# Kernel tuning notes

Measured on AMD Instinct MI355X. Metric: run time of the kernel, lower is better.

The kernel has to match this reference:

```python
import jax, jax.numpy as jnp
import numpy as np

EPS = 1e-5
PDIM, QKD, DIM = 64, 16, 256
SCALE = QKD ** -0.5


def setup_inputs() -> dict:
    key = jax.random.key(0)
    ks = jax.random.split(key, 13)
    B, H, W = 8, 64, 64
    return {
        "x": jax.random.normal(ks[0], (B, DIM, H, W), jnp.float32),
        "gn_g": jax.random.uniform(ks[1], (PDIM,), jnp.float32, 0.5, 1.5),
        "gn_b": jax.random.normal(ks[2], (PDIM,), jnp.float32) * 0.1,
        "qkv_w": jax.random.normal(ks[3], (2 * QKD + PDIM, PDIM), jnp.float32) * (PDIM ** -0.5),
        "qkv_bn_g": jax.random.uniform(ks[4], (2 * QKD + PDIM,), jnp.float32, 0.5, 1.5),
        "qkv_bn_b": jax.random.normal(ks[5], (2 * QKD + PDIM,), jnp.float32) * 0.1,
        "qkv_rm": jax.random.normal(ks[6], (2 * QKD + PDIM,), jnp.float32) * 0.1,
        "qkv_rv": jax.random.uniform(ks[7], (2 * QKD + PDIM,), jnp.float32, 0.5, 1.5),
        "proj_w": jax.random.normal(ks[8], (DIM, DIM), jnp.float32) * (DIM ** -0.5),
        "proj_bn_g": jax.random.uniform(ks[9], (DIM,), jnp.float32, 0.5, 1.5),
        "proj_bn_b": jax.random.normal(ks[10], (DIM,), jnp.float32) * 0.1,
        "proj_rm": jax.random.normal(ks[11], (DIM,), jnp.float32) * 0.1,
        "proj_rv": jax.random.uniform(ks[12], (DIM,), jnp.float32, 0.5, 1.5),
    }


def _bn(y, g, b, rm, rv):
    # inference BatchNorm over channel axis 1 of [B,C,H,W]
    inv = g / jnp.sqrt(rv + EPS)
    return y * inv[None, :, None, None] + (b - rm * inv)[None, :, None, None]


def reference(x, gn_g, gn_b, qkv_w, qkv_bn_g, qkv_bn_b, qkv_rm, qkv_rv,
              proj_w, proj_bn_g, proj_bn_b, proj_rm, proj_rv):
    B, C, H, W = x.shape
    x1, x2 = x[:, :PDIM], x[:, PDIM:]
    # GroupNorm with 1 group: normalize over (C,H,W) per sample
    mu = jnp.mean(x1, axis=(1, 2, 3), keepdims=True)
    var = jnp.var(x1, axis=(1, 2, 3), keepdims=True)
    x1n = (x1 - mu) / jnp.sqrt(var + EPS)
    x1n = x1n * gn_g[None, :, None, None] + gn_b[None, :, None, None]
    # qkv: 1x1 conv + BN
    qkv = jnp.einsum('bchw,oc->bohw', x1n, qkv_w)
    qkv = _bn(qkv, qkv_bn_g, qkv_bn_b, qkv_rm, qkv_rv)
    q, k, v = qkv[:, :QKD], qkv[:, QKD:2 * QKD], qkv[:, 2 * QKD:]
    N = H * W
    q = q.reshape(B, QKD, N)
    k = k.reshape(B, QKD, N)
    v = v.reshape(B, PDIM, N)
    attn = jnp.einsum('bcn,bcm->bnm', q, k) * SCALE  # [B,N,N]
    attn = jax.nn.softmax(attn, axis=-1)
    x1_attn = jnp.einsum('bcm,bnm->bcn', v, attn).reshape(B, PDIM, H, W)
    xc = jnp.concatenate([x1_attn, x2], axis=1)
    # proj: ReLU -> 1x1 conv -> BN
    y = jnp.einsum('bchw,oc->bohw', jax.nn.relu(xc), proj_w)
    return _bn(y, proj_bn_g, proj_bn_b, proj_rm, proj_rv)
```

## Files before the change

kernel.cpp:

```cpp
#include <hip/hip_runtime.h>
#include <hip/hip_bf16.h>

typedef __bf16 bf16;
typedef __bf16 bf16x4 __attribute__((ext_vector_type(4)));
typedef __bf16 bf16x8 __attribute__((ext_vector_type(8)));
typedef float  f32x16 __attribute__((ext_vector_type(16)));

#define MFMA32 __builtin_amdgcn_mfma_f32_32x32x16_bf16
#define EPSV 1e-5f
#define QSCALE 0.36067376022224085f

__device__ __forceinline__ f32x16 fzero16() {
  f32x16 z;
#pragma unroll
  for (int i = 0; i < 16; ++i) z[i] = 0.f;
  return z;
}

__global__ __launch_bounds__(256) void k_stats_partial(const float* __restrict__ x,
                                                       float* __restrict__ part) {
  const int b = blockIdx.x >> 5, k = blockIdx.x & 31;
  const float* p = x + (size_t)b * 256 * 4096 + k * 8192;
  const int t = threadIdx.x;
  float s = 0.f, q = 0.f;
#pragma unroll
  for (int j = 0; j < 8; ++j) {
    float4 v = ((const float4*)p)[t + j * 256];
    s += v.x + v.y + v.z + v.w;
    q += v.x * v.x + v.y * v.y + v.z * v.z + v.w * v.w;
  }
  __shared__ float ls[256], lq[256];
  ls[t] = s; lq[t] = q;
  __syncthreads();
  for (int off = 128; off > 0; off >>= 1) {
    if (t < off) { ls[t] += ls[t + off]; lq[t] += lq[t + off]; }
    __syncthreads();
  }
  if (t == 0) { part[blockIdx.x * 2] = ls[0]; part[blockIdx.x * 2 + 1] = lq[0]; }
}

__global__ __launch_bounds__(256) void k_stats_final(const float* __restrict__ part,
                                                     float* __restrict__ stats) {
  const int t = threadIdx.x, b = t >> 5, k = t & 31;
  float s = part[(b * 32 + k) * 2], q = part[(b * 32 + k) * 2 + 1];
  for (int off = 16; off > 0; off >>= 1) {
    s += __shfl_down(s, off, 32);
    q += __shfl_down(q, off, 32);
  }
  if (k == 0) {
    const float inv_n = 1.f / 262144.f;
    const float mu = s * inv_n;
    const float var = q * inv_n - mu * mu;
    stats[b * 2] = mu;
    stats[b * 2 + 1] = rsqrtf(var + EPSV);
  }
}

__global__ __launch_bounds__(256) void k_qkv(
    const float* __restrict__ x, const float* __restrict__ gn_g, const float* __restrict__ gn_b,
    const float* __restrict__ qkv_w, const float* __restrict__ bn_g, const float* __restrict__ bn_b,
    const float* __restrict__ bn_rm, const float* __restrict__ bn_rv,
    const float* __restrict__ stats,
    bf16* __restrict__ qw, bf16* __restrict__ kw, bf16* __restrict__ vw) {
  const int b = blockIdx.x >> 6, tile = blockIdx.x & 63;
  const int n0 = tile * 64, t = threadIdx.x;
  __shared__ float xn[64][68];
  __shared__ float W[64][96];
  __shared__ float beta_s[96];
  const float mu = stats[b * 2], rstd = stats[b * 2 + 1];
  {
    const int c = t >> 2, f = t & 3;
    const float A = rstd * gn_g[c], B = gn_b[c] - mu * A;
    const float* xr = x + ((size_t)b * 256 + c) * 4096 + n0;
#pragma unroll
    for (int j = 0; j < 4; ++j) {
      float4 v = ((const float4*)xr)[f * 4 + j];
      const int nb = f * 16 + j * 4;
      xn[c][nb + 0] = v.x * A + B; xn[c][nb + 1] = v.y * A + B;
      xn[c][nb + 2] = v.z * A + B; xn[c][nb + 3] = v.w * A + B;
    }
  }
  for (int oc = t; oc < 96 * 8; oc += 256) {
    const int o = oc >> 3, ch = (oc & 7) * 8;
    const float inv = bn_g[o] * rsqrtf(bn_rv[o] + EPSV);
    if (ch == 0) beta_s[o] = bn_b[o] - bn_rm[o] * inv;
    const float* wr = qkv_w + o * 64 + ch;
#pragma unroll
    for (int i = 0; i < 8; ++i) W[ch + i][o] = wr[i] * inv;
  }
  __syncthreads();
  const int o_l = t & 31, ng = t >> 5;
#pragma unroll 1
  for (int p = 0; p < 3; ++p) {
    const int o = p * 32 + o_l;
    float acc[8];
#pragma unroll
    for (int j = 0; j < 8; ++j) acc[j] = 0.f;
    for (int c = 0; c < 64; ++c) {
      const float wv = W[c][o];
      const float* xr = &xn[c][ng * 8];
#pragma unroll
      for (int j = 0; j < 8; ++j) acc[j] += wv * xr[j];
    }
    const float beta = beta_s[o];
    const int nb = n0 + ng * 8;
    if (p == 0) {
      if (o < 16) {
#pragma unroll
        for (int j = 0; j < 8; ++j)
          qw[((size_t)b * 4096 + nb + j) * 16 + o] = (bf16)((acc[j] + beta) * QSCALE);
      } else {
#pragma unroll
        for (int j = 0; j < 8; ++j)
          kw[((size_t)b * 4096 + nb + j) * 16 + (o - 16)] = (bf16)(acc[j] + beta);
      }
    } else {
      const int c = (p - 1) * 32 + o_l;
      bf16* vr = vw + ((size_t)b * 64 + c) * 4096 + nb;
#pragma unroll
      for (int q4 = 0; q4 < 2; ++q4) {
        bf16x4 pk;
        pk[0] = (bf16)(acc[q4 * 4 + 0] + beta); pk[1] = (bf16)(acc[q4 * 4 + 1] + beta);
        pk[2] = (bf16)(acc[q4 * 4 + 2] + beta); pk[3] = (bf16)(acc[q4 * 4 + 3] + beta);
        *(bf16x4*)(vr + q4 * 4) = pk;
      }
    }
  }
}

__global__ __launch_bounds__(1024, 4) void k_attn(
    const bf16* __restrict__ qw, const bf16* __restrict__ kw,
    const bf16* __restrict__ vw, const float* __restrict__ x,
    bf16* __restrict__ xc) {
  __shared__ __align__(16) char smem[81920];
  const int orig = blockIdx.x;
  const int wg = (orig & 7) * 32 + (orig >> 3);
  const int b = wg >> 5, qt = wg & 31;
  const int t = threadIdx.x;
  const int grp = t >> 8, tg = t & 255;
  const int wv4 = tg >> 6, l = t & 63, ln = l & 31, g = l >> 5;

  const bf16* qb = qw + (size_t)b * 4096 * 16;
  const char* kb = (const char*)(kw + (size_t)b * 4096 * 16);
  const bf16* vb = vw + (size_t)b * 64 * 4096;
  const int m0 = grp * 1024;

  char* kbase = smem + grp * 4096;
  char* vbase = smem + 16384 + grp * 16384;

  const char* ksrc = kb + (size_t)m0 * 32 + tg * 8;
  const int klds = (((tg >> 1) & 1) << 10) + ((tg >> 2) << 4) + ((tg & 1) << 3);
  const int vc = tg >> 2, vq = tg & 3;
  const bf16* vsrc = vb + (size_t)vc * 4096 + m0 + vq * 16;
  const int vswz = (vc & 15) * 8;

  const bf16x8 qf = *(const bf16x8*)(qb + (size_t)(qt * 128 + wv4 * 32 + ln) * 16 + g * 8);

  uint2 kr = *(const uint2*)ksrc;
  uint4 vr0 = *(const uint4*)vsrc;
  uint4 vr1 = *(const uint4*)(vsrc + 8);
  *(uint2*)(kbase + klds) = kr;
  {
    char* vrow = vbase + vc * 128;
    *(uint2*)(vrow + ((vq * 32 +  0) ^ vswz)) = make_uint2(vr0.x, vr0.y);
    *(uint2*)(vrow + ((vq * 32 +  8) ^ vswz)) = make_uint2(vr0.z, vr0.w);
    *(uint2*)(vrow + ((vq * 32 + 16) ^ vswz)) = make_uint2(vr1.x, vr1.y);
    *(uint2*)(vrow + ((vq * 32 + 24) ^ vswz)) = make_uint2(vr1.z, vr1.w);
  }
  __syncthreads();

  f32x16 O0 = fzero16(), O1 = fzero16();
  float l_run = 0.f;
  const int vsw = (ln & 15) * 8;

  int p = 0;
#pragma unroll 1
  for (int it = 0; it < 16; ++it) {
    if (it + 1 < 16) {
      kr  = *(const uint2*)(ksrc + (size_t)(it + 1) * 2048);
      vr0 = *(const uint4*)(vsrc + (it + 1) * 64);
      vr1 = *(const uint4*)(vsrc + (it + 1) * 64 + 8);
    }
    const bf16x8 kf0 = *(const bf16x8*)(kbase + p * 2048 + g * 1024 + ln * 16);
    const bf16x8 kf1 = *(const bf16x8*)(kbase + p * 2048 + g * 1024 + (ln + 32) * 16);
    f32x16 S0 = MFMA32(kf0, qf, fzero16(), 0, 0, 0);
    f32x16 S1 = MFMA32(kf1, qf, fzero16(), 0, 0, 0);
    float ts = 0.f;
#pragma unroll
    for (int r = 0; r < 16; ++r) { S0[r] = __builtin_amdgcn_exp2f(S0[r]); ts += S0[r]; }
#pragma unroll
    for (int r = 0; r < 16; ++r) { S1[r] = __builtin_amdgcn_exp2f(S1[r]); ts += S1[r]; }
    ts += __shfl_xor(ts, 32, 64);
    l_run += ts;
    bf16x8 pb0, pb1, pb2, pb3;
#pragma unroll
    for (int r = 0; r < 8; ++r) {
      pb0[r] = (bf16)S0[r]; pb1[r] = (bf16)S0[r + 8];
      pb2[r] = (bf16)S1[r]; pb3[r] = (bf16)S1[r + 8];
    }
    {
      const char* rlo = vbase + p * 8192 + ln * 128;
      const char* rhi = vbase + p * 8192 + (ln + 32) * 128;
#pragma unroll
      for (int kg = 0; kg < 4; ++kg) {
        const int c0 = (kg * 32 + 8 * g) ^ vsw;
        const int c1 = (kg * 32 + 16 + 8 * g) ^ vsw;
        bf16x4 lo = *(const bf16x4*)(rlo + c0);
        bf16x4 hi = *(const bf16x4*)(rlo + c1);
        bf16x8 va = __builtin_shufflevector(lo, hi, 0, 1, 2, 3, 4, 5, 6, 7);
        const bf16x8 pb = kg == 0 ? pb0 : kg == 1 ? pb1 : kg == 2 ? pb2 : pb3;
        O0 = MFMA32(va, pb, O0, 0, 0, 0);
        lo = *(const bf16x4*)(rhi + c0);
        hi = *(const bf16x4*)(rhi + c1);
        va = __builtin_shufflevector(lo, hi, 0, 1, 2, 3, 4, 5, 6, 7);
        O1 = MFMA32(va, pb, O1, 0, 0, 0);
      }
    }
    if (it + 1 < 16) {
      *(uint2*)(kbase + (p ^ 1) * 2048 + klds) = kr;
      char* vrow = vbase + (p ^ 1) * 8192 + vc * 128;
      *(uint2*)(vrow + ((vq * 32 +  0) ^ vswz)) = make_uint2(vr0.x, vr0.y);
      *(uint2*)(vrow + ((vq * 32 +  8) ^ vswz)) = make_uint2(vr0.z, vr0.w);
      *(uint2*)(vrow + ((vq * 32 + 16) ^ vswz)) = make_uint2(vr1.x, vr1.y);
      *(uint2*)(vrow + ((vq * 32 + 24) ^ vswz)) = make_uint2(vr1.z, vr1.w);
    }
    __syncthreads();
    p ^= 1;
  }

  {
    const int nl = wv4 * 32 + ln;
    char* orow = smem + 16384 + grp * 16384 + nl * 128;
    const int xr = (nl & 7) << 4;
#pragma unroll
    for (int h = 0; h < 2; ++h) {
      const f32x16& O = h ? O1 : O0;
#pragma unroll
      for (int q4 = 0; q4 < 4; ++q4) {
        bf16x4 e;
#pragma unroll
        for (int i = 0; i < 4; ++i) e[i] = (bf16)O[q4 * 4 + i];
        *(bf16x4*)(orow + ((h * 64 + q4 * 16 + g * 8) ^ xr)) = e;
      }
    }
    if (g == 0) *(float*)(smem + grp * 4096 + nl * 4) = l_run;
  }
  __syncthreads();
  {
    const int n8 = t >> 3, o8 = t & 7;
    const int xr = (n8 & 7) << 4;
    float L = 0.f;
    float acc[8];
#pragma unroll
    for (int e = 0; e < 8; ++e) acc[e] = 0.f;
#pragma unroll
    for (int gr = 0; gr < 4; ++gr) {
      L += *(const float*)(smem + gr * 4096 + n8 * 4);
      const bf16x8 v = *(const bf16x8*)(smem + 16384 + gr * 16384 + n8 * 128 +
                                        ((o8 * 16) ^ xr));
#pragma unroll
      for (int e = 0; e < 8; ++e) acc[e] += (float)v[e];
    }
    const float rL = 1.0f / L;
    bf16x8 o;
#pragma unroll
    for (int e = 0; e < 8; ++e) o[e] = (bf16)fmaxf(acc[e] * rL, 0.f);
    *(bf16x8*)(xc + ((size_t)b * 4096 + qt * 128 + n8) * 256 + o8 * 8) = o;
  }
  __syncthreads();

  {
    unsigned* tile_u = (unsigned*)smem;
    const float* xb = x + ((size_t)b * 256 + 64) * 4096 + qt * 128;
#pragma unroll
    for (int i = 0; i < 3; ++i) {
      const int idx = i * 1024 + t;
      const int cp = idx >> 5, f = idx & 31;
      const float4 a = *(const float4*)(xb + (size_t)(2 * cp) * 4096 + f * 4);
      const float4 c4 = *(const float4*)(xb + (size_t)(2 * cp + 1) * 4096 + f * 4);
      const float av[4] = {a.x, a.y, a.z, a.w};
      const float cv[4] = {c4.x, c4.y, c4.z, c4.w};
#pragma unroll
      for (int e = 0; e < 4; ++e) {
        const unsigned u =
            (unsigned)__builtin_bit_cast(unsigned short, (bf16)fmaxf(av[e], 0.f)) |
            ((unsigned)__builtin_bit_cast(unsigned short, (bf16)fmaxf(cv[e], 0.f)) << 16);
        tile_u[(f * 4 + e) * 100 + cp] = u;
      }
    }
    __syncthreads();
#pragma unroll
    for (int i = 0; i < 3; ++i) {
      const int idx = i * 1024 + t;
      const int n = idx / 24, q = idx % 24;
      const uint4 d = *(const uint4*)&tile_u[n * 100 + q * 4];
      *(uint4*)(xc + ((size_t)b * 4096 + qt * 128 + n) * 256 + 64 + q * 8) = d;
    }
  }
}

__global__ __launch_bounds__(256, 2) void k_proj(
    const bf16* __restrict__ xc, const float* __restrict__ pw,
    const float* __restrict__ bn_g, const float* __restrict__ bn_b,
    const float* __restrict__ bn_rm, const float* __restrict__ bn_rv,
    float* __restrict__ out) {
  const int orig = blockIdx.x;
  const int wg = (orig & 7) * 64 + (orig >> 3);
  const int b = wg >> 6, rem = wg & 63, nt = rem >> 1, oh = rem & 1;
  const int n0 = nt * 128, o0 = oh * 128;
  const int t = threadIdx.x, w = t >> 6, l = t & 63, ln = l & 31, g = l >> 5;

  __shared__ __align__(16) bf16 pws[128 * 256];
  __shared__ float beta_s[128];

  {
    const int o = t >> 1, half = t & 1;
    const float inv = bn_g[o0 + o] * rsqrtf(bn_rv[o0 + o] + EPSV);
    if (half == 0) beta_s[o] = bn_b[o0 + o] - bn_rm[o0 + o] * inv;
    const float* wr = pw + (size_t)(o0 + o) * 256 + half * 128;
    const int s_hh = (o & 15) * 8;
#pragma unroll
    for (int j = 0; j < 16; ++j) {
      const float4 a = ((const float4*)wr)[j * 2];
      const float4 c4 = ((const float4*)wr)[j * 2 + 1];
      bf16x8 v8;
      v8[0] = (bf16)(a.x * inv);  v8[1] = (bf16)(a.y * inv);
      v8[2] = (bf16)(a.z * inv);  v8[3] = (bf16)(a.w * inv);
      v8[4] = (bf16)(c4.x * inv); v8[5] = (bf16)(c4.y * inv);
      v8[6] = (bf16)(c4.z * inv); v8[7] = (bf16)(c4.w * inv);
      *(bf16x8*)&pws[o * 256 + ((half * 128 + j * 8) ^ s_hh)] = v8;
    }
  }
  __syncthreads();

  const bf16* xrow = xc + ((size_t)b * 4096 + n0 + w * 32 + ln) * 256;
  const int sw = (ln & 15) * 8;
  f32x16 acc0 = fzero16(), acc1 = fzero16(), acc2 = fzero16(), acc3 = fzero16();
#pragma unroll 4
  for (int ck = 0; ck < 256; ck += 16) {
    const bf16x8 bfrag = *(const bf16x8*)(xrow + ck + g * 8);
    const int cidx = (ck + g * 8) ^ sw;
    const bf16x8 a0 = *(const bf16x8*)&pws[(ln) * 256 + cidx];
    const bf16x8 a1 = *(const bf16x8*)&pws[(32 + ln) * 256 + cidx];
    const bf16x8 a2 = *(const bf16x8*)&pws[(64 + ln) * 256 + cidx];
    const bf16x8 a3 = *(const bf16x8*)&pws[(96 + ln) * 256 + cidx];
    acc0 = MFMA32(a0, bfrag, acc0, 0, 0, 0);
    acc1 = MFMA32(a1, bfrag, acc1, 0, 0, 0);
    acc2 = MFMA32(a2, bfrag, acc2, 0, 0, 0);
    acc3 = MFMA32(a3, bfrag, acc3, 0, 0, 0);
  }
  const int ncol = n0 + w * 32 + ln;
  float* ob = out + (size_t)b * 256 * 4096 + ncol;
#pragma unroll
  for (int og = 0; og < 4; ++og) {
    const f32x16& A = og == 0 ? acc0 : og == 1 ? acc1 : og == 2 ? acc2 : acc3;
#pragma unroll
    for (int r = 0; r < 16; ++r) {
      const int o_loc = og * 32 + (r & 3) + 8 * (r >> 2) + 4 * g;
      ob[(size_t)(o0 + o_loc) * 4096] = A[r] + beta_s[o_loc];
    }
  }
}

extern "C" void kernel_launch(void* const* d_in, const int* in_sizes, int n_in,
                              void* d_out, int out_size, void* d_ws, size_t ws_size,
                              hipStream_t stream) {
  (void)in_sizes; (void)n_in; (void)out_size; (void)ws_size;
  const float* x        = (const float*)d_in[0];
  const float* gn_g     = (const float*)d_in[1];
  const float* gn_b     = (const float*)d_in[2];
  const float* qkv_w    = (const float*)d_in[3];
  const float* qkv_bn_g = (const float*)d_in[4];
  const float* qkv_bn_b = (const float*)d_in[5];
  const float* qkv_rm   = (const float*)d_in[6];
  const float* qkv_rv   = (const float*)d_in[7];
  const float* proj_w   = (const float*)d_in[8];
  const float* proj_bn_g = (const float*)d_in[9];
  const float* proj_bn_b = (const float*)d_in[10];
  const float* proj_rm  = (const float*)d_in[11];
  const float* proj_rv  = (const float*)d_in[12];

  char* ws = (char*)d_ws;
  float* part  = (float*)ws;
  float* stats = (float*)(ws + 4096);
  bf16* qw = (bf16*)(ws + 8192);
  bf16* kw = (bf16*)(ws + 8192 + (1u << 20));
  bf16* vw = (bf16*)(ws + 8192 + (2u << 20));
  bf16* xc = (bf16*)(ws + 8192 + (6u << 20));

  k_stats_partial<<<256, 256, 0, stream>>>(x, part);
  k_stats_final<<<1, 256, 0, stream>>>(part, stats);
  k_qkv<<<512, 256, 0, stream>>>(x, gn_g, gn_b, qkv_w, qkv_bn_g, qkv_bn_b,
                                 qkv_rm, qkv_rv, stats, qw, kw, vw);
  k_attn<<<256, 1024, 0, stream>>>(qw, kw, vw, x, xc);
  k_proj<<<512, 256, 0, stream>>>(xc, proj_w, proj_bn_g, proj_bn_b,
                                  proj_rm, proj_rv, (float*)d_out);
}
```

Baseline: 90.62 us.

## Restructure attention into wave-private key/value pipelines with smaller blocks

Result: slower. 123.3 us (+36.0%).

```diff
diff --git a/kernel.cpp b/kernel.cpp
--- a/kernel.cpp
+++ b/kernel.cpp
@@ -128,154 +128,143 @@
   }
 }
 
-__global__ __launch_bounds__(1024, 4) void k_attn(
+__global__ __launch_bounds__(512, 4) void k_attn(
     const bf16* __restrict__ qw, const bf16* __restrict__ kw,
     const bf16* __restrict__ vw, const float* __restrict__ x,
     bf16* __restrict__ xc) {
-  __shared__ __align__(16) char smem[81920];
+  __shared__ __align__(16) char smem[40960];
   const int orig = blockIdx.x;
-  const int wg = (orig & 7) * 32 + (orig >> 3);
-  const int b = wg >> 5, qt = wg & 31;
+  const int wg = (orig & 7) * 64 + (orig >> 3);
+  const int b = wg >> 6, qblk = wg & 63;
   const int t = threadIdx.x;
-  const int grp = t >> 8, tg = t & 255;
-  const int wv4 = tg >> 6, l = t & 63, ln = l & 31, g = l >> 5;
+  const int wid = t >> 6, l = t & 63, ln = l & 31, g = l >> 5;
+  const int qsub = wid & 1, kr = wid >> 1;
 
   const bf16* qb = qw + (size_t)b * 4096 * 16;
   const char* kb = (const char*)(kw + (size_t)b * 4096 * 16);
   const bf16* vb = vw + (size_t)b * 64 * 4096;
-  const int m0 = grp * 1024;
-
-  char* kbase = smem + grp * 4096;
-  char* vbase = smem + 16384 + grp * 16384;
-
-  const char* ksrc = kb + (size_t)m0 * 32 + tg * 8;
-  const int klds = (((tg >> 1) & 1) << 10) + ((tg >> 2) << 4) + ((tg & 1) << 3);
-  const int vc = tg >> 2, vq = tg & 3;
-  const bf16* vsrc = vb + (size_t)vc * 4096 + m0 + vq * 16;
-  const int vswz = (vc & 15) * 8;
-
-  const bf16x8 qf = *(const bf16x8*)(qb + (size_t)(qt * 128 + wv4 * 32 + ln) * 16 + g * 8);
-
-  uint2 kr = *(const uint2*)ksrc;
-  uint4 vr0 = *(const uint4*)vsrc;
-  uint4 vr1 = *(const uint4*)(vsrc + 8);
-  *(uint2*)(kbase + klds) = kr;
-  {
-    char* vrow = vbase + vc * 128;
-    *(uint2*)(vrow + ((vq * 32 +  0) ^ vswz)) = make_uint2(vr0.x, vr0.y);
-    *(uint2*)(vrow + ((vq * 32 +  8) ^ vswz)) = make_uint2(vr0.z, vr0.w);
-    *(uint2*)(vrow + ((vq * 32 + 16) ^ vswz)) = make_uint2(vr1.x, vr1.y);
-    *(uint2*)(vrow + ((vq * 32 + 24) ^ vswz)) = make_uint2(vr1.z, vr1.w);
-  }
-  __syncthreads();
+  const int m0 = kr * 1024;
+
+  char* kbuf = smem + wid * 1024;
+  char* vbuf = smem + 8192 + wid * 4096;
+
+  const char* ksrc = kb + (size_t)m0 * 32 + l * 16;
+  const bf16* vsrc = vb + (size_t)l * 4096 + m0;
+  const int vxw = l & 3;
+  const int kwaddr = l * 16;
+  const int vwa0 = l * 64 + ((0 ^ vxw) << 4);
+  const int vwa1 = l * 64 + ((1 ^ vxw) << 4);
+  const int vwa2 = l * 64 + ((2 ^ vxw) << 4);
+  const int vwa3 = l * 64 + ((3 ^ vxw) << 4);
+
+  const int nq = qblk * 64 + qsub * 32 + ln;
+  const bf16x8 qf = *(const bf16x8*)(qb + (size_t)nq * 16 + g * 8);
 
   f32x16 O0 = fzero16(), O1 = fzero16();
   float l_run = 0.f;
-  const int vsw = (ln & 15) * 8;
-
-  int p = 0;
+
+  uint4 kreg = *(const uint4*)ksrc;
+  uint4 sv0 = *(const uint4*)(vsrc);
+  uint4 sv1 = *(const uint4*)(vsrc + 8);
+  uint4 sv2 = *(const uint4*)(vsrc + 16);
+  uint4 sv3 = *(const uint4*)(vsrc + 24);
+  *(uint4*)(kbuf + kwaddr) = kreg;
+  *(uint4*)(vbuf + vwa0) = make_uint4(sv0.x, sv0.y, sv1.x, sv1.y);
+  *(uint4*)(vbuf + vwa1) = make_uint4(sv0.z, sv0.w, sv1.z, sv1.w);
+  *(uint4*)(vbuf + vwa2) = make_uint4(sv2.x, sv2.y, sv3.x, sv3.y);
+  *(uint4*)(vbuf + vwa3) = make_uint4(sv2.z, sv2.w, sv3.z, sv3.w);
+  kreg = *(const uint4*)(ksrc + 1024);
+  sv0 = *(const uint4*)(vsrc + 32);
+  sv1 = *(const uint4*)(vsrc + 40);
+  sv2 = *(const uint4*)(vsrc + 48);
+  sv3 = *(const uint4*)(vsrc + 56);
+
 #pragma unroll 1
-  for (int it = 0; it < 16; ++it) {
-    if (it + 1 < 16) {
-      kr  = *(const uint2*)(ksrc + (size_t)(it + 1) * 2048);
-      vr0 = *(const uint4*)(vsrc + (it + 1) * 64);
-      vr1 = *(const uint4*)(vsrc + (it + 1) * 64 + 8);
-    }
-    const bf16x8 kf0 = *(const bf16x8*)(kbase + p * 2048 + g * 1024 + ln * 16);
-    const bf16x8 kf1 = *(const bf16x8*)(kbase + p * 2048 + g * 1024 + (ln + 32) * 16);
-    f32x16 S0 = MFMA32(kf0, qf, fzero16(), 0, 0, 0);
-    f32x16 S1 = MFMA32(kf1, qf, fzero16(), 0, 0, 0);
+  for (int it = 0; it < 32; ++it) {
+    const bf16x8 kf = *(const bf16x8*)(kbuf + ln * 32 + g * 16);
+    f32x16 S = MFMA32(kf, qf, fzero16(), 0, 0, 0);
     float ts = 0.f;
 #pragma unroll
-    for (int r = 0; r < 16; ++r) { S0[r] = __builtin_amdgcn_exp2f(S0[r]); ts += S0[r]; }
-#pragma unroll
-    for (int r = 0; r < 16; ++r) { S1[r] = __builtin_amdgcn_exp2f(S1[r]); ts += S1[r]; }
+    for (int r = 0; r < 16; ++r) { S[r] = __builtin_amdgcn_exp2f(S[r]); ts += S[r]; }
     ts += __shfl_xor(ts, 32, 64);
     l_run += ts;
-    bf16x8 pb0, pb1, pb2, pb3;
-#pragma unroll
-    for (int r = 0; r < 8; ++r) {
-      pb0[r] = (bf16)S0[r]; pb1[r] = (bf16)S0[r + 8];
-      pb2[r] = (bf16)S1[r]; pb3[r] = (bf16)S1[r + 8];
-    }
-    {
-      const char* rlo = vbase + p * 8192 + ln * 128;
-      const char* rhi = vbase + p * 8192 + (ln + 32) * 128;
-#pragma unroll
-      for (int kg = 0; kg < 4; ++kg) {
-        const int c0 = (kg * 32 + 8 * g) ^ vsw;
-        const int c1 = (kg * 32 + 16 + 8 * g) ^ vsw;
-        bf16x4 lo = *(const bf16x4*)(rlo + c0);
-        bf16x4 hi = *(const bf16x4*)(rlo + c1);
-        bf16x8 va = __builtin_shufflevector(lo, hi, 0, 1, 2, 3, 4, 5, 6, 7);
-        const bf16x8 pb = kg == 0 ? pb0 : kg == 1 ? pb1 : kg == 2 ? pb2 : pb3;
-        O0 = MFMA32(va, pb, O0, 0, 0, 0);
-        lo = *(const bf16x4*)(rhi + c0);
-        hi = *(const bf16x4*)(rhi + c1);
-        va = __builtin_shufflevector(lo, hi, 0, 1, 2, 3, 4, 5, 6, 7);
-        O1 = MFMA32(va, pb, O1, 0, 0, 0);
-      }
-    }
-    if (it + 1 < 16) {
-      *(uint2*)(kbase + (p ^ 1) * 2048 + klds) = kr;
-      char* vrow = vbase + (p ^ 1) * 8192 + vc * 128;
-      *(uint2*)(vrow + ((vq * 32 +  0) ^ vswz)) = make_uint2(vr0.x, vr0.y);
-      *(uint2*)(vrow + ((vq * 32 +  8) ^ vswz)) = make_uint2(vr0.z, vr0.w);
-      *(uint2*)(vrow + ((vq * 32 + 16) ^ vswz)) = make_uint2(vr1.x, vr1.y);
-      *(uint2*)(vrow + ((vq * 32 + 24) ^ vswz)) = make_uint2(vr1.z, vr1.w);
-    }
-    __syncthreads();
-    p ^= 1;
-  }
-
-  {
-    const int nl = wv4 * 32 + ln;
-    char* orow = smem + 16384 + grp * 16384 + nl * 128;
-    const int xr = (nl & 7) << 4;
+    bf16x8 pb0, pb1;
+#pragma unroll
+    for (int r = 0; r < 8; ++r) { pb0[r] = (bf16)S[r]; pb1[r] = (bf16)S[r + 8]; }
+#pragma unroll
+    for (int kb_ = 0; kb_ < 2; ++kb_) {
+      const bf16x8 pb = kb_ ? pb1 : pb0;
+      const int gsel = ((kb_ * 2 + g) ^ (ln & 3)) << 4;
+      const bf16x8 vf0 = *(const bf16x8*)(vbuf + ln * 64 + gsel);
+      O0 = MFMA32(vf0, pb, O0, 0, 0, 0);
+      const bf16x8 vf1 = *(const bf16x8*)(vbuf + (ln + 32) * 64 + gsel);
+      O1 = MFMA32(vf1, pb, O1, 0, 0, 0);
+    }
+    if (it + 1 < 32) {
+      *(uint4*)(kbuf + kwaddr) = kreg;
+      *(uint4*)(vbuf + vwa0) = make_uint4(sv0.x, sv0.y, sv1.x, sv1.y);
+      *(uint4*)(vbuf + vwa1) = make_uint4(sv0.z, sv0.w, sv1.z, sv1.w);
+      *(uint4*)(vbuf + vwa2) = make_uint4(sv2.x, sv2.y, sv3.x, sv3.y);
+      *(uint4*)(vbuf + vwa3) = make_uint4(sv2.z, sv2.w, sv3.z, sv3.w);
+      if (it + 2 < 32) {
+        kreg = *(const uint4*)(ksrc + (size_t)(it + 2) * 1024);
+        sv0 = *(const uint4*)(vsrc + (it + 2) * 32);
+        sv1 = *(const uint4*)(vsrc + (it + 2) * 32 + 8);
+        sv2 = *(const uint4*)(vsrc + (it + 2) * 32 + 16);
+        sv3 = *(const uint4*)(vsrc + (it + 2) * 32 + 24);
+      }
+    }
+  }
+
+  {
+    const int msk = 2 * (ln & 7);
 #pragma unroll
     for (int h = 0; h < 2; ++h) {
       const f32x16& O = h ? O1 : O0;
 #pragma unroll
-      for (int q4 = 0; q4 < 4; ++q4) {
+      for (int j = 0; j < 4; ++j) {
         bf16x4 e;
 #pragma unroll
-        for (int i = 0; i < 4; ++i) e[i] = (bf16)O[q4 * 4 + i];
-        *(bf16x4*)(orow + ((h * 64 + q4 * 16 + g * 8) ^ xr)) = e;
-      }
-    }
-    if (g == 0) *(float*)(smem + grp * 4096 + nl * 4) = l_run;
-  }
-  __syncthreads();
-  {
-    const int n8 = t >> 3, o8 = t & 7;
-    const int xr = (n8 & 7) << 4;
+        for (int i = 0; i < 4; ++i) e[i] = (bf16)O[4 * j + i];
+        const int chunk = h * 8 + 2 * j + g;
+        *(bf16x4*)(vbuf + ln * 128 + ((chunk ^ msk) << 3)) = e;
+      }
+    }
+    if (g == 0) *(float*)(kbuf + ln * 4) = l_run;
+  }
+  __syncthreads();
+
+  {
+    const int qs = t >> 8, tt = t & 255;
+    const int n = tt >> 3, k8 = tt & 7;
     float L = 0.f;
     float acc[8];
 #pragma unroll
     for (int e = 0; e < 8; ++e) acc[e] = 0.f;
 #pragma unroll
-    for (int gr = 0; gr < 4; ++gr) {
-      L += *(const float*)(smem + gr * 4096 + n8 * 4);
-      const bf16x8 v = *(const bf16x8*)(smem + 16384 + gr * 16384 + n8 * 128 +
-                                        ((o8 * 16) ^ xr));
+    for (int kr_ = 0; kr_ < 4; ++kr_) {
+      const int wsrc = kr_ * 2 + qs;
+      L += *(const float*)(smem + wsrc * 1024 + n * 4);
+      const bf16x8 v = *(const bf16x8*)(smem + 8192 + wsrc * 4096 + n * 128 +
+                                        (((2 * k8) ^ (2 * (n & 7))) << 3));
 #pragma unroll
       for (int e = 0; e < 8; ++e) acc[e] += (float)v[e];
     }
     const float rL = 1.0f / L;
-    bf16x8 o;
-#pragma unroll
-    for (int e = 0; e < 8; ++e) o[e] = (bf16)fmaxf(acc[e] * rL, 0.f);
-    *(bf16x8*)(xc + ((size_t)b * 4096 + qt * 128 + n8) * 256 + o8 * 8) = o;
+    bf16x8 o8;
+#pragma unroll
+    for (int e = 0; e < 8; ++e) o8[e] = (bf16)fmaxf(acc[e] * rL, 0.f);
+    *(bf16x8*)(xc + ((size_t)b * 4096 + qblk * 64 + qs * 32 + n) * 256 + k8 * 8) = o8;
   }
   __syncthreads();
 
   {
     unsigned* tile_u = (unsigned*)smem;
-    const float* xb = x + ((size_t)b * 256 + 64) * 4096 + qt * 128;
+    const float* xb = x + ((size_t)b * 256 + 64) * 4096 + qblk * 64;
 #pragma unroll
     for (int i = 0; i < 3; ++i) {
-      const int idx = i * 1024 + t;
-      const int cp = idx >> 5, f = idx & 31;
+      const int idx = i * 512 + t;
+      const int cp = idx >> 4, f = idx & 15;
       const float4 a = *(const float4*)(xb + (size_t)(2 * cp) * 4096 + f * 4);
       const float4 c4 = *(const float4*)(xb + (size_t)(2 * cp + 1) * 4096 + f * 4);
       const float av[4] = {a.x, a.y, a.z, a.w};
@@ -285,16 +274,16 @@
         const unsigned u =
             (unsigned)__builtin_bit_cast(unsigned short, (bf16)fmaxf(av[e], 0.f)) |
             ((unsigned)__builtin_bit_cast(unsigned short, (bf16)fmaxf(cv[e], 0.f)) << 16);
-        tile_u[(f * 4 + e) * 100 + cp] = u;
+        tile_u[(f * 4 + e) * 97 + cp] = u;
       }
     }
     __syncthreads();
 #pragma unroll
     for (int i = 0; i < 3; ++i) {
-      const int idx = i * 1024 + t;
+      const int idx = i * 512 + t;
       const int n = idx / 24, q = idx % 24;
-      const uint4 d = *(const uint4*)&tile_u[n * 100 + q * 4];
-      *(uint4*)(xc + ((size_t)b * 4096 + qt * 128 + n) * 256 + 64 + q * 8) = d;
+      const uint4 d = *(const uint4*)&tile_u[n * 97 + q * 4];
+      *(uint4*)(xc + ((size_t)b * 4096 + qblk * 64 + n) * 256 + 64 + q * 8) = d;
     }
   }
 }
@@ -392,7 +381,7 @@
   k_stats_final<<<1, 256, 0, stream>>>(part, stats);
   k_qkv<<<512, 256, 0, stream>>>(x, gn_g, gn_b, qkv_w, qkv_bn_g, qkv_bn_b,
                                  qkv_rm, qkv_rv, stats, qw, kw, vw);
-  k_attn<<<256, 1024, 0, stream>>>(qw, kw, vw, x, xc);
+  k_attn<<<512, 512, 0, stream>>>(qw, kw, vw, x, xc);
   k_proj<<<512, 256, 0, stream>>>(xc, proj_w, proj_bn_g, proj_bn_b,
                                   proj_rm, proj_rv, (float*)d_out);
 }
```
